# Kernel tuning notes

Hardware: AMD Instinct MI355X
Metric: run time of the kernel (lower is better)

Reference implementation:

```python
import jax, jax.numpy as jnp
import numpy as np

D, H, COND, MLP_RATIO = 1024, 16, 1024, 4
HD = D // H
DFF = MLP_RATIO * D


def layer_norm(x, w, eps=1e-5):
    xf = x.astype(jnp.float32)
    mu = jnp.mean(xf, axis=-1, keepdims=True)
    var = jnp.mean((xf - mu) ** 2, axis=-1, keepdims=True)
    return (xf - mu) * jax.lax.rsqrt(var + eps) * w


def rms_norm(x, w, eps=1e-6):
    xf = x.astype(jnp.float32)
    rms = jnp.sqrt(jnp.mean(xf * xf, axis=-1, keepdims=True) + eps)
    return (xf / rms * w).astype(x.dtype)


def rotate_half(x):
    x1, x2 = x[..., : x.shape[-1] // 2], x[..., x.shape[-1] // 2:]
    return jnp.concatenate([-x2, x1], axis=-1)


def apply_rope(x, cos, sin):
    return x * cos + rotate_half(x) * sin


def setup_inputs() -> dict:
    key = jax.random.key(0)
    ks = jax.random.split(key, 16)
    B, S = 4, 2048
    pos = jnp.arange(S, dtype=jnp.float32)
    inv = 1.0 / (10000.0 ** (jnp.arange(0, HD, 2, dtype=jnp.float32) / HD))
    freqs = pos[:, None] * inv[None, :]              # (S, HD/2)
    emb = jnp.concatenate([freqs, freqs], axis=-1)   # (S, HD)
    return {
        "x": jax.random.normal(ks[0], (B, S, D), jnp.float32),
        "cos": jnp.cos(emb)[None, :, None, :],        # (1,S,1,HD)
        "sin": jnp.sin(emb)[None, :, None, :],
        "c": jax.random.normal(ks[1], (B, COND), jnp.float32),
        "norm1_w": jnp.ones((D,), jnp.float32),
        "Wqkv": jax.random.normal(ks[2], (D, 3 * D), jnp.float32) * 0.02,
        "Wout": jax.random.normal(ks[3], (D, D), jnp.float32) * 0.02,
        "q_norm_w": jnp.ones((HD,), jnp.float32),
        "k_norm_w": jnp.ones((HD,), jnp.float32),
        "norm2_w": jnp.ones((D,), jnp.float32),
        "W1": jax.random.normal(ks[4], (D, DFF), jnp.float32) * 0.02,
        "b1": jnp.zeros((DFF,), jnp.float32),
        "W2": jax.random.normal(ks[5], (DFF, D), jnp.float32) * 0.02,
        "b2": jnp.zeros((D,), jnp.float32),
        "ada_W": jax.random.normal(ks[6], (COND, 6 * D), jnp.float32) * 0.02,
        "ada_b": jnp.zeros((6 * D,), jnp.float32),
    }


def reference(x, cos, sin, c, norm1_w, Wqkv, Wout, q_norm_w, k_norm_w,
              norm2_w, W1, b1, W2, b2, ada_W, ada_b):
    B, S, _ = x.shape
    mod = (c @ ada_W + ada_b)[:, None, :]            # (B,1,6D)
    sh_msa, sc_msa, g_msa, sh_mlp, sc_mlp, g_mlp = jnp.split(mod, 6, axis=-1)

    x_norm = layer_norm(x, norm1_w) * (1 + sc_msa) + sh_msa
    qkv = (x_norm @ Wqkv).reshape(B, S, 3, H, HD)
    q, k, v = qkv[:, :, 0], qkv[:, :, 1], qkv[:, :, 2]  # (B,S,H,HD)
    q = apply_rope(rms_norm(q, q_norm_w), cos, sin)
    k = apply_rope(rms_norm(k, k_norm_w), cos, sin)

    scale = 1.0 / jnp.sqrt(jnp.float32(HD))
    logits = jnp.einsum('bqhd,bkhd->bhqk', q, k) * scale
    probs = jax.nn.softmax(logits, axis=-1)
    attn = jnp.einsum('bhqk,bkhd->bqhd', probs, v).reshape(B, S, D)

    x = x + g_msa * (attn @ Wout)

    x_norm = layer_norm(x, norm2_w) * (1 + sc_mlp) + sh_mlp
    h = jax.nn.gelu(x_norm @ W1 + b1, approximate=True)
    x = x + g_mlp * (h @ W2 + b2)
    return x
```

## Files before the change

kernel.cpp:

```cpp
#include <hip/hip_runtime.h>
#include <hip/hip_bf16.h>
#include <math.h>

typedef __bf16 bf16;
typedef __bf16 bf16x8 __attribute__((ext_vector_type(8)));
typedef __bf16 bf16x4 __attribute__((ext_vector_type(4)));
typedef float f32x4 __attribute__((ext_vector_type(4)));
typedef short s16x4 __attribute__((ext_vector_type(4)));

#define S_LEN 2048
#define NTOK 8192
#define DIM 1024
#define NH 16
#define HEADD 64
#define DFF 4096
#define MODD 6144

__device__ __forceinline__ void gload_lds16(const bf16* g, bf16* l) {
  __builtin_amdgcn_global_load_lds(
      (const __attribute__((address_space(1))) void*)g,
      (__attribute__((address_space(3))) void*)l, 16, 0, 0);
}

__device__ __forceinline__ float gelu_tanh(float x) {
  float inner = 0.7978845608028654f * (x + 0.044715f * x * x * x);
  return 0.5f * x * (1.0f + tanhf(inner));
}

__global__ __launch_bounds__(256) void init_mod_kernel(
    const float* __restrict__ ada_b, float* __restrict__ mod) {
  int i = blockIdx.x * 256 + threadIdx.x;
  mod[i] = ada_b[i % MODD];
}

__global__ __launch_bounds__(256) void ada_gemm_kernel(
    const float* __restrict__ cnd, const float* __restrict__ W,
    float* __restrict__ mod) {
  int n = blockIdx.x * 256 + threadIdx.x;
  int k0 = blockIdx.y * 128;
  float a0 = 0.f, a1 = 0.f, a2 = 0.f, a3 = 0.f;
  for (int k = k0; k < k0 + 128; ++k) {
    float w = W[(size_t)k * MODD + n];
    a0 = fmaf(cnd[k], w, a0);
    a1 = fmaf(cnd[1024 + k], w, a1);
    a2 = fmaf(cnd[2048 + k], w, a2);
    a3 = fmaf(cnd[3072 + k], w, a3);
  }
  atomicAdd(&mod[n], a0);
  atomicAdd(&mod[MODD + n], a1);
  atomicAdd(&mod[2 * MODD + n], a2);
  atomicAdd(&mod[3 * MODD + n], a3);
}

__global__ __launch_bounds__(256) void transpose_cast_kernel(
    const float* __restrict__ W, bf16* __restrict__ Wt, int K, int N) {
  __shared__ float tile[32][33];
  int n0 = blockIdx.x * 32, k0 = blockIdx.y * 32;
  int r = threadIdx.x >> 3;
  int c4 = (threadIdx.x & 7) * 4;
  float4 v = *(const float4*)&W[(size_t)(k0 + r) * N + n0 + c4];
  tile[r][c4 + 0] = v.x; tile[r][c4 + 1] = v.y;
  tile[r][c4 + 2] = v.z; tile[r][c4 + 3] = v.w;
  __syncthreads();
  bf16x4 o;
  o[0] = (bf16)tile[c4 + 0][r];
  o[1] = (bf16)tile[c4 + 1][r];
  o[2] = (bf16)tile[c4 + 2][r];
  o[3] = (bf16)tile[c4 + 3][r];
  *(bf16x4*)&Wt[(size_t)(n0 + r) * K + k0 + c4] = o;
}

__global__ __launch_bounds__(256) void vtrans_kernel(
    const bf16* __restrict__ qkv, bf16* __restrict__ VT) {
  __shared__ __align__(16) bf16 t[64][72];
  const int bh = blockIdx.y;
  const int b = bh >> 4, h = bh & 15;
  const int s0 = blockIdx.x * 64;
  const int tid = threadIdx.x;
  {
    const int r = tid >> 2;
    const int c = (tid & 3) * 16;
    const bf16* src =
        qkv + (size_t)(b * S_LEN + s0 + r) * 3072 + 2048 + h * 64 + c;
    *(bf16x8*)&t[r][c] = *(const bf16x8*)src;
    *(bf16x8*)&t[r][c + 8] = *(const bf16x8*)(src + 8);
  }
  __syncthreads();
  {
    const int d = tid & 63;
    const int sc = (tid >> 6) * 16;
    bf16x8 o0, o1;
#pragma unroll
    for (int j = 0; j < 8; ++j) o0[j] = t[sc + j][d];
#pragma unroll
    for (int j = 0; j < 8; ++j) o1[j] = t[sc + 8 + j][d];
    bf16* dst = VT + (size_t)(bh * 64 + d) * S_LEN + s0 + sc;
    *(bf16x8*)dst = o0;
    *(bf16x8*)(dst + 8) = o1;
  }
}

__global__ __launch_bounds__(256) void ln_mod_kernel(
    const float* __restrict__ x, const float* __restrict__ w,
    const float* __restrict__ mod, int sh_off, int sc_off,
    bf16* __restrict__ out) {
  __shared__ float red[8];
  const int row = blockIdx.x;
  const int b = row >> 11;
  const int tid = threadIdx.x;
  const float4 v = ((const float4*)(x + (size_t)row * DIM))[tid];
  float s1 = v.x + v.y + v.z + v.w;
  float s2 = v.x * v.x + v.y * v.y + v.z * v.z + v.w * v.w;
  for (int off = 32; off > 0; off >>= 1) {
    s1 += __shfl_down(s1, off, 64);
    s2 += __shfl_down(s2, off, 64);
  }
  const int wid = tid >> 6;
  if ((tid & 63) == 0) { red[wid] = s1; red[4 + wid] = s2; }
  __syncthreads();
  s1 = red[0] + red[1] + red[2] + red[3];
  s2 = red[4] + red[5] + red[6] + red[7];
  const float mu = s1 * (1.0f / DIM);
  const float inv = rsqrtf(s2 * (1.0f / DIM) - mu * mu + 1e-5f);
  const int c = tid * 4;
  const float* mb = mod + (size_t)b * MODD;
  float xs[4] = {v.x, v.y, v.z, v.w};
  bf16x4 o;
#pragma unroll
  for (int j = 0; j < 4; ++j)
    o[j] = (bf16)(((xs[j] - mu) * inv) * w[c + j] * (1.0f + mb[sc_off + c + j]) +
                  mb[sh_off + c + j]);
  *(bf16x4*)(out + (size_t)row * DIM + c) = o;
}

template <int EPI>
__global__ __launch_bounds__(256) void gemm_bt(
    const bf16* __restrict__ A, const bf16* __restrict__ Bt,
    bf16* __restrict__ Cb, float* __restrict__ Cf,
    const float* __restrict__ bias, const float* __restrict__ gmod,
    const float* __restrict__ resid, int M, int N, int K) {
  __shared__ __align__(16) bf16 As[2][128 * 32];
  __shared__ __align__(16) bf16 Bs[2][128 * 32];
  const int tid = threadIdx.x;
  const int wid = tid >> 6;
  const int lane = tid & 63;
  const int l15 = lane & 15;
  const int quad = lane >> 4;
  const int m0 = blockIdx.y * 128;
  const int n0 = blockIdx.x * 128;
  const int wm = (wid & 1) * 64;
  const int wn = (wid >> 1) * 64;

  const int r0 = tid >> 2;
  const int cc0 = (tid & 3) * 8;
  const size_t a_base = (size_t)(m0 + r0) * K + cc0;
  const size_t a_base2 = (size_t)(m0 + 64 + r0) * K + cc0;
  const size_t b_base = (size_t)(n0 + r0) * K + cc0;
  const size_t b_base2 = (size_t)(n0 + 64 + r0) * K + cc0;

  f32x4 acc[4][4] = {};

  for (int kt = 0; kt < K; kt += 64) {
    gload_lds16(A + a_base + kt, &As[0][tid * 8]);
    gload_lds16(A + a_base2 + kt, &As[0][(256 + tid) * 8]);
    gload_lds16(Bt + b_base + kt, &Bs[0][tid * 8]);
    gload_lds16(Bt + b_base2 + kt, &Bs[0][(256 + tid) * 8]);
    gload_lds16(A + a_base + kt + 32, &As[1][tid * 8]);
    gload_lds16(A + a_base2 + kt + 32, &As[1][(256 + tid) * 8]);
    gload_lds16(Bt + b_base + kt + 32, &Bs[1][tid * 8]);
    gload_lds16(Bt + b_base2 + kt + 32, &Bs[1][(256 + tid) * 8]);
    __syncthreads();
#pragma unroll
    for (int half = 0; half < 2; ++half) {
      bf16x8 af[4], bfr[4];
#pragma unroll
      for (int i = 0; i < 4; ++i) {
        af[i] = *(const bf16x8*)&As[half][(wm + i * 16 + l15) * 32 + quad * 8];
        bfr[i] = *(const bf16x8*)&Bs[half][(wn + i * 16 + l15) * 32 + quad * 8];
      }
#pragma unroll
      for (int i = 0; i < 4; ++i)
#pragma unroll
        for (int j = 0; j < 4; ++j)
          acc[i][j] = __builtin_amdgcn_mfma_f32_16x16x32_bf16(af[i], bfr[j],
                                                              acc[i][j], 0, 0, 0);
    }
    __syncthreads();
  }

#pragma unroll
  for (int i = 0; i < 4; ++i) {
#pragma unroll
    for (int r = 0; r < 4; ++r) {
      const int m = m0 + wm + i * 16 + quad * 4 + r;
#pragma unroll
      for (int j = 0; j < 4; ++j) {
        const int n = n0 + wn + j * 16 + l15;
        float v = acc[i][j][r];
        if (EPI == 0) {
          Cb[(size_t)m * N + n] = (bf16)v;
        } else if (EPI == 1) {
          const int b = m >> 11;
          Cf[(size_t)m * N + n] =
              resid[(size_t)m * N + n] + gmod[(size_t)b * MODD + n] * v;
        } else if (EPI == 2) {
          v += bias[n];
          Cb[(size_t)m * N + n] = (bf16)gelu_tanh(v);
        } else {
          v += bias[n];
          const int b = m >> 11;
          Cf[(size_t)m * N + n] =
              resid[(size_t)m * N + n] + gmod[(size_t)b * MODD + n] * v;
        }
      }
    }
  }
}

__global__ __launch_bounds__(256) void rope_kernel(
    bf16* __restrict__ qkv, const float* __restrict__ cosb,
    const float* __restrict__ sinb, const float* __restrict__ qw,
    const float* __restrict__ kw) {
  const int wid = threadIdx.x >> 6;
  const int lane = threadIdx.x & 63;
  const int inst = blockIdx.x * 4 + wid;
  const int h = inst & (NH - 1);
  const int token = inst >> 4;
  const int s = token & (S_LEN - 1);
  const size_t base = (size_t)token * (3 * DIM) + h * HEADD + lane;
  const float cv = cosb[s * HEADD + lane];
  const float sv = sinb[s * HEADD + lane];
  const float sign = (lane < 32) ? -1.0f : 1.0f;
  {
    float xq = (float)qkv[base];
    float ss = xq * xq;
    for (int off = 1; off < 64; off <<= 1) ss += __shfl_xor(ss, off, 64);
    float rn = rsqrtf(ss * (1.0f / HEADD) + 1e-6f);
    float xn = xq * rn * qw[lane];
    float other = __shfl_xor(xn, 32, 64);
    qkv[base] = (bf16)(xn * cv + sign * other * sv);
  }
  {
    float xk = (float)qkv[base + DIM];
    float ss = xk * xk;
    for (int off = 1; off < 64; off <<= 1) ss += __shfl_xor(ss, off, 64);
    float rn = rsqrtf(ss * (1.0f / HEADD) + 1e-6f);
    float xn = xk * rn * kw[lane];
    float other = __shfl_xor(xn, 32, 64);
    qkv[base + DIM] = (bf16)(xn * cv + sign * other * sv);
  }
}

__global__ __launch_bounds__(256) void attn_kernel(
    const bf16* __restrict__ qkv, const bf16* __restrict__ VT,
    bf16* __restrict__ out) {
  __shared__ __align__(16) bf16 Ks[4096];
  __shared__ __align__(16) bf16 Vs[4096];
  const int bh = blockIdx.y;
  const int b = bh >> 4;
  const int h = bh & 15;
  const int q0 = blockIdx.x * 128;
  const int tid = threadIdx.x;
  const int wid = tid >> 6;
  const int lane = tid & 63;
  const int l15 = lane & 15;
  const int quad = lane >> 4;

  bf16x8 aq[2][2];
#pragma unroll
  for (int i = 0; i < 2; ++i) {
    const int qrow = q0 + wid * 32 + i * 16 + l15;
    const size_t qbase = (size_t)(b * S_LEN + qrow) * (3 * DIM) + h * HEADD;
    aq[i][0] = *(const bf16x8*)(qkv + qbase + quad * 8);
    aq[i][1] = *(const bf16x8*)(qkv + qbase + 32 + quad * 8);
  }

  const int rstage = tid & 63;
  const int kbase = tid >> 6;
  const float cexp = 0.125f * 1.44269504f;

  f32x4 oacc[2][4] = {};
  float psum[2] = {0.f, 0.f};

  for (int kt = 0; kt < S_LEN; kt += 64) {
    __syncthreads();
    const bf16* krow = qkv + (size_t)(b * S_LEN + kt + rstage) * 3072 + DIM + h * HEADD;
    const bf16* vrow = VT + (size_t)(bh * 64 + rstage) * S_LEN + kt;
    const int rsw = rstage & 7;
#pragma unroll
    for (int rr = 0; rr < 2; ++rr) {
      const int ck = kbase + 4 * rr;
      const int sw = ((ck ^ rsw) << 3);
      *(bf16x8*)&Ks[rstage * 64 + sw] = *(const bf16x8*)(krow + ck * 8);
      *(bf16x8*)&Vs[rstage * 64 + sw] = *(const bf16x8*)(vrow + ck * 8);
    }
    __syncthreads();

    f32x4 sc[2][4] = {};
#pragma unroll
    for (int hh = 0; hh < 2; ++hh) {
#pragma unroll
      for (int cc = 0; cc < 4; ++cc) {
        const int row = cc * 16 + l15;
        const bf16x8 kf = *(const bf16x8*)&Ks[row * 64 + (((quad + 4 * hh) ^ (l15 & 7)) << 3)];
#pragma unroll
        for (int i = 0; i < 2; ++i)
          sc[i][cc] = __builtin_amdgcn_mfma_f32_16x16x32_bf16(kf, aq[i][hh],
                                                              sc[i][cc], 0, 0, 0);
      }
    }

    s16x4 pf[2][4];
#pragma unroll
    for (int i = 0; i < 2; ++i)
#pragma unroll
      for (int cc = 0; cc < 4; ++cc) {
        bf16x4 pb;
#pragma unroll
        for (int r = 0; r < 4; ++r) {
          const float p = __builtin_amdgcn_exp2f(fmaf(sc[i][cc][r], cexp, -8.0f));
          psum[i] += p;
          pb[r] = (bf16)p;
        }
        pf[i][cc] = __builtin_bit_cast(s16x4, pb);
      }

#pragma unroll
    for (int j = 0; j < 4; ++j) {
      const int d = 16 * j + l15;
      const int drow = d * 64;
      const int dsw = d & 7;
#pragma unroll
      for (int cc = 0; cc < 4; ++cc) {
        const int ck = 2 * cc + (quad >> 1);
        const s16x4 vf = *(const s16x4*)&Vs[drow + ((ck ^ dsw) << 3) + ((quad & 1) << 2)];
#pragma unroll
        for (int i = 0; i < 2; ++i)
          oacc[i][j] = __builtin_amdgcn_mfma_f32_16x16x16bf16_1k(pf[i][cc], vf,
                                                                 oacc[i][j], 0, 0, 0);
      }
    }
  }

#pragma unroll
  for (int i = 0; i < 2; ++i) {
    float ps = psum[i];
    ps += __shfl_xor(ps, 16, 64);
    ps += __shfl_xor(ps, 32, 64);
#pragma unroll
    for (int r = 0; r < 4; ++r) {
      const float invl = 1.0f / __shfl(ps, quad * 4 + r, 64);
      const int m = q0 + wid * 32 + i * 16 + quad * 4 + r;
#pragma unroll
      for (int j = 0; j < 4; ++j)
        out[((size_t)(b * S_LEN + m) * NH + h) * HEADD + j * 16 + l15] =
            (bf16)(oacc[i][j][r] * invl);
    }
  }
}

extern "C" void kernel_launch(void* const* d_in, const int* in_sizes, int n_in,
                              void* d_out, int out_size, void* d_ws,
                              size_t ws_size, hipStream_t stream) {
  const float* x = (const float*)d_in[0];
  const float* cosb = (const float*)d_in[1];
  const float* sinb = (const float*)d_in[2];
  const float* cnd = (const float*)d_in[3];
  const float* norm1_w = (const float*)d_in[4];
  const float* Wqkv = (const float*)d_in[5];
  const float* Wout = (const float*)d_in[6];
  const float* q_norm_w = (const float*)d_in[7];
  const float* k_norm_w = (const float*)d_in[8];
  const float* norm2_w = (const float*)d_in[9];
  const float* W1 = (const float*)d_in[10];
  const float* b1 = (const float*)d_in[11];
  const float* W2 = (const float*)d_in[12];
  const float* b2 = (const float*)d_in[13];
  const float* ada_W = (const float*)d_in[14];
  const float* ada_b = (const float*)d_in[15];
  float* out = (float*)d_out;

  char* p = (char*)d_ws;
  float* mod = (float*)p;   p += (size_t)4 * MODD * 4;
  bf16* WqkvT = (bf16*)p;   p += (size_t)3072 * 1024 * 2;
  bf16* WoutT = (bf16*)p;   p += (size_t)1024 * 1024 * 2;
  bf16* W1T = (bf16*)p;     p += (size_t)4096 * 1024 * 2;
  bf16* W2T = (bf16*)p;     p += (size_t)1024 * 4096 * 2;
  bf16* XN = (bf16*)p;      p += (size_t)NTOK * DIM * 2;
  bf16* QKV = (bf16*)p;     p += (size_t)NTOK * 3 * DIM * 2;
  bf16* ATTN = (bf16*)p;    p += (size_t)NTOK * DIM * 2;
  bf16* Hbuf = (bf16*)p;    p += (size_t)NTOK * DFF * 2;
  bf16* VT = Hbuf;

  init_mod_kernel<<<96, 256, 0, stream>>>(ada_b, mod);
  ada_gemm_kernel<<<dim3(24, 8), 256, 0, stream>>>(cnd, ada_W, mod);
  transpose_cast_kernel<<<dim3(96, 32), 256, 0, stream>>>(Wqkv, WqkvT, 1024, 3072);
  transpose_cast_kernel<<<dim3(32, 32), 256, 0, stream>>>(Wout, WoutT, 1024, 1024);
  transpose_cast_kernel<<<dim3(128, 32), 256, 0, stream>>>(W1, W1T, 1024, 4096);
  transpose_cast_kernel<<<dim3(32, 128), 256, 0, stream>>>(W2, W2T, 4096, 1024);
  ln_mod_kernel<<<NTOK, 256, 0, stream>>>(x, norm1_w, mod, 0, 1024, XN);
  gemm_bt<0><<<dim3(24, 64), 256, 0, stream>>>(XN, WqkvT, QKV, nullptr, nullptr,
                                               nullptr, nullptr, NTOK, 3072, 1024);
  rope_kernel<<<NTOK * NH / 4, 256, 0, stream>>>(QKV, cosb, sinb, q_norm_w, k_norm_w);
  vtrans_kernel<<<dim3(32, 64), 256, 0, stream>>>(QKV, VT);
  attn_kernel<<<dim3(16, 64), 256, 0, stream>>>(QKV, VT, ATTN);
  gemm_bt<1><<<dim3(8, 64), 256, 0, stream>>>(ATTN, WoutT, nullptr, out, nullptr,
                                              mod + 2 * 1024, x, NTOK, 1024, 1024);
  ln_mod_kernel<<<NTOK, 256, 0, stream>>>(out, norm2_w, mod, 3 * 1024, 4 * 1024, XN);
  gemm_bt<2><<<dim3(32, 64), 256, 0, stream>>>(XN, W1T, Hbuf, nullptr, b1, nullptr,
                                               nullptr, NTOK, DFF, 1024);
  gemm_bt<3><<<dim3(8, 64), 256, 0, stream>>>(Hbuf, W2T, nullptr, out, b2,
                                              mod + 5 * 1024, out, NTOK, 1024, DFF);
  (void)in_sizes; (void)n_in; (void)out_size; (void)ws_size;
}
```

Before: 681.4 us.

## Fuse QK-norm and RoPE into QKV GEMM, split-K attention, 64-row tiles for N=1024 GEMMs

Moves the per-head RMS norm and RoPE into the QKV GEMM epilogue, which removes the separate rope kernel and its read-modify-write pass over Q/K. Attention is split into two key halves run as separate blocks, with the next K/V tile prefetched into registers. A new reduce kernel sums the unnormalised partial outputs and softmax sums. The Wout and W2 GEMMs use 64-row M tiles to launch more blocks. Partial outputs are stored in bf16 without max subtraction, so precision and scratch traffic both add cost and risk.

```diff
diff --git a/kernel.cpp b/kernel.cpp
--- a/kernel.cpp
+++ b/kernel.cpp
@@ -133,22 +133,25 @@
   *(bf16x4*)(out + (size_t)row * DIM + c) = o;
 }
 
-template <int EPI>
+template <int EPI, int MT>
 __global__ __launch_bounds__(256) void gemm_bt(
     const bf16* __restrict__ A, const bf16* __restrict__ Bt,
     bf16* __restrict__ Cb, float* __restrict__ Cf,
     const float* __restrict__ bias, const float* __restrict__ gmod,
-    const float* __restrict__ resid, int M, int N, int K) {
-  __shared__ __align__(16) bf16 As[2][128 * 32];
+    const float* __restrict__ resid, const float* __restrict__ cosb,
+    const float* __restrict__ sinb, const float* __restrict__ qw,
+    const float* __restrict__ kw, int M, int N, int K) {
+  constexpr int IM = MT / 32;
+  __shared__ __align__(16) bf16 As[2][MT * 32];
   __shared__ __align__(16) bf16 Bs[2][128 * 32];
   const int tid = threadIdx.x;
   const int wid = tid >> 6;
   const int lane = tid & 63;
   const int l15 = lane & 15;
   const int quad = lane >> 4;
-  const int m0 = blockIdx.y * 128;
+  const int m0 = blockIdx.y * MT;
   const int n0 = blockIdx.x * 128;
-  const int wm = (wid & 1) * 64;
+  const int wm = (wid & 1) * (MT / 2);
   const int wn = (wid >> 1) * 64;
 
   const int r0 = tid >> 2;
@@ -158,28 +161,29 @@
   const size_t b_base = (size_t)(n0 + r0) * K + cc0;
   const size_t b_base2 = (size_t)(n0 + 64 + r0) * K + cc0;
 
-  f32x4 acc[4][4] = {};
+  f32x4 acc[IM][4] = {};
 
   for (int kt = 0; kt < K; kt += 64) {
     gload_lds16(A + a_base + kt, &As[0][tid * 8]);
-    gload_lds16(A + a_base2 + kt, &As[0][(256 + tid) * 8]);
+    if (MT == 128) gload_lds16(A + a_base2 + kt, &As[0][(256 + tid) * 8]);
     gload_lds16(Bt + b_base + kt, &Bs[0][tid * 8]);
     gload_lds16(Bt + b_base2 + kt, &Bs[0][(256 + tid) * 8]);
     gload_lds16(A + a_base + kt + 32, &As[1][tid * 8]);
-    gload_lds16(A + a_base2 + kt + 32, &As[1][(256 + tid) * 8]);
+    if (MT == 128) gload_lds16(A + a_base2 + kt + 32, &As[1][(256 + tid) * 8]);
     gload_lds16(Bt + b_base + kt + 32, &Bs[1][tid * 8]);
     gload_lds16(Bt + b_base2 + kt + 32, &Bs[1][(256 + tid) * 8]);
     __syncthreads();
 #pragma unroll
     for (int half = 0; half < 2; ++half) {
-      bf16x8 af[4], bfr[4];
-#pragma unroll
-      for (int i = 0; i < 4; ++i) {
+      bf16x8 af[IM], bfr[4];
+#pragma unroll
+      for (int i = 0; i < IM; ++i)
         af[i] = *(const bf16x8*)&As[half][(wm + i * 16 + l15) * 32 + quad * 8];
-        bfr[i] = *(const bf16x8*)&Bs[half][(wn + i * 16 + l15) * 32 + quad * 8];
-      }
-#pragma unroll
-      for (int i = 0; i < 4; ++i)
+#pragma unroll
+      for (int j = 0; j < 4; ++j)
+        bfr[j] = *(const bf16x8*)&Bs[half][(wn + j * 16 + l15) * 32 + quad * 8];
+#pragma unroll
+      for (int i = 0; i < IM; ++i)
 #pragma unroll
         for (int j = 0; j < 4; ++j)
           acc[i][j] = __builtin_amdgcn_mfma_f32_16x16x32_bf16(af[i], bfr[j],
@@ -188,8 +192,43 @@
     __syncthreads();
   }
 
-#pragma unroll
-  for (int i = 0; i < 4; ++i) {
+  if (EPI == 4 && n0 < 2048) {
+    const float* nw = ((n0 + wn) < 1024) ? qw : kw;
+    float wv[4];
+#pragma unroll
+    for (int j = 0; j < 4; ++j) wv[j] = nw[j * 16 + l15];
+#pragma unroll
+    for (int i = 0; i < IM; ++i) {
+#pragma unroll
+      for (int r = 0; r < 4; ++r) {
+        const int m = m0 + wm + i * 16 + quad * 4 + r;
+        const int s = m & (S_LEN - 1);
+        float v[4];
+        float ss = 0.f;
+#pragma unroll
+        for (int j = 0; j < 4; ++j) { v[j] = acc[i][j][r]; ss += v[j] * v[j]; }
+        ss += __shfl_xor(ss, 1, 64);
+        ss += __shfl_xor(ss, 2, 64);
+        ss += __shfl_xor(ss, 4, 64);
+        ss += __shfl_xor(ss, 8, 64);
+        const float inv = rsqrtf(ss * (1.0f / HEADD) + 1e-6f);
+        float xn[4];
+#pragma unroll
+        for (int j = 0; j < 4; ++j) xn[j] = v[j] * inv * wv[j];
+#pragma unroll
+        for (int j = 0; j < 4; ++j) {
+          const int d = j * 16 + l15;
+          const float rot = (j < 2) ? -xn[j + 2] : xn[j - 2];
+          const float o = xn[j] * cosb[s * HEADD + d] + rot * sinb[s * HEADD + d];
+          Cb[(size_t)m * N + n0 + wn + d] = (bf16)o;
+        }
+      }
+    }
+    return;
+  }
+
+#pragma unroll
+  for (int i = 0; i < IM; ++i) {
 #pragma unroll
     for (int r = 0; r < 4; ++r) {
       const int m = m0 + wm + i * 16 + quad * 4 + r;
@@ -197,7 +236,7 @@
       for (int j = 0; j < 4; ++j) {
         const int n = n0 + wn + j * 16 + l15;
         float v = acc[i][j][r];
-        if (EPI == 0) {
+        if (EPI == 0 || EPI == 4) {
           Cb[(size_t)m * N + n] = (bf16)v;
         } else if (EPI == 1) {
           const int b = m >> 11;
@@ -217,49 +256,16 @@
   }
 }
 
-__global__ __launch_bounds__(256) void rope_kernel(
-    bf16* __restrict__ qkv, const float* __restrict__ cosb,
-    const float* __restrict__ sinb, const float* __restrict__ qw,
-    const float* __restrict__ kw) {
-  const int wid = threadIdx.x >> 6;
-  const int lane = threadIdx.x & 63;
-  const int inst = blockIdx.x * 4 + wid;
-  const int h = inst & (NH - 1);
-  const int token = inst >> 4;
-  const int s = token & (S_LEN - 1);
-  const size_t base = (size_t)token * (3 * DIM) + h * HEADD + lane;
-  const float cv = cosb[s * HEADD + lane];
-  const float sv = sinb[s * HEADD + lane];
-  const float sign = (lane < 32) ? -1.0f : 1.0f;
-  {
-    float xq = (float)qkv[base];
-    float ss = xq * xq;
-    for (int off = 1; off < 64; off <<= 1) ss += __shfl_xor(ss, off, 64);
-    float rn = rsqrtf(ss * (1.0f / HEADD) + 1e-6f);
-    float xn = xq * rn * qw[lane];
-    float other = __shfl_xor(xn, 32, 64);
-    qkv[base] = (bf16)(xn * cv + sign * other * sv);
-  }
-  {
-    float xk = (float)qkv[base + DIM];
-    float ss = xk * xk;
-    for (int off = 1; off < 64; off <<= 1) ss += __shfl_xor(ss, off, 64);
-    float rn = rsqrtf(ss * (1.0f / HEADD) + 1e-6f);
-    float xn = xk * rn * kw[lane];
-    float other = __shfl_xor(xn, 32, 64);
-    qkv[base + DIM] = (bf16)(xn * cv + sign * other * sv);
-  }
-}
-
 __global__ __launch_bounds__(256) void attn_kernel(
     const bf16* __restrict__ qkv, const bf16* __restrict__ VT,
-    bf16* __restrict__ out) {
+    bf16* __restrict__ Opart, float* __restrict__ psumbuf) {
   __shared__ __align__(16) bf16 Ks[4096];
   __shared__ __align__(16) bf16 Vs[4096];
   const int bh = blockIdx.y;
   const int b = bh >> 4;
   const int h = bh & 15;
   const int q0 = blockIdx.x * 128;
+  const int split = blockIdx.z;
   const int tid = threadIdx.x;
   const int wid = tid >> 6;
   const int lane = tid & 63;
@@ -275,26 +281,44 @@
     aq[i][1] = *(const bf16x8*)(qkv + qbase + 32 + quad * 8);
   }
 
-  const int rstage = tid & 63;
-  const int kbase = tid >> 6;
+  const int rstage = lane;
+  const int rsw = rstage & 7;
+  const bf16* krow =
+      qkv + (size_t)(b * S_LEN + split * 1024 + rstage) * 3072 + DIM + h * HEADD;
+  const bf16* vrow = VT + (size_t)(bh * 64 + rstage) * S_LEN + split * 1024;
+
+  bf16x8 kreg[2], vreg[2];
+#pragma unroll
+  for (int rr = 0; rr < 2; ++rr) {
+    const int ck = wid + 4 * rr;
+    kreg[rr] = *(const bf16x8*)(krow + ck * 8);
+    vreg[rr] = *(const bf16x8*)(vrow + ck * 8);
+  }
+
   const float cexp = 0.125f * 1.44269504f;
-
   f32x4 oacc[2][4] = {};
   float psum[2] = {0.f, 0.f};
 
-  for (int kt = 0; kt < S_LEN; kt += 64) {
+  for (int t = 0; t < 16; ++t) {
     __syncthreads();
-    const bf16* krow = qkv + (size_t)(b * S_LEN + kt + rstage) * 3072 + DIM + h * HEADD;
-    const bf16* vrow = VT + (size_t)(bh * 64 + rstage) * S_LEN + kt;
-    const int rsw = rstage & 7;
 #pragma unroll
     for (int rr = 0; rr < 2; ++rr) {
-      const int ck = kbase + 4 * rr;
+      const int ck = wid + 4 * rr;
       const int sw = ((ck ^ rsw) << 3);
-      *(bf16x8*)&Ks[rstage * 64 + sw] = *(const bf16x8*)(krow + ck * 8);
-      *(bf16x8*)&Vs[rstage * 64 + sw] = *(const bf16x8*)(vrow + ck * 8);
+      *(bf16x8*)&Ks[rstage * 64 + sw] = kreg[rr];
+      *(bf16x8*)&Vs[rstage * 64 + sw] = vreg[rr];
     }
     __syncthreads();
+    if (t < 15) {
+      krow += 64 * 3072;
+      vrow += 64;
+#pragma unroll
+      for (int rr = 0; rr < 2; ++rr) {
+        const int ck = wid + 4 * rr;
+        kreg[rr] = *(const bf16x8*)(krow + ck * 8);
+        vreg[rr] = *(const bf16x8*)(vrow + ck * 8);
+      }
+    }
 
     f32x4 sc[2][4] = {};
 #pragma unroll
@@ -302,7 +326,8 @@
 #pragma unroll
       for (int cc = 0; cc < 4; ++cc) {
         const int row = cc * 16 + l15;
-        const bf16x8 kf = *(const bf16x8*)&Ks[row * 64 + (((quad + 4 * hh) ^ (l15 & 7)) << 3)];
+        const bf16x8 kf =
+            *(const bf16x8*)&Ks[row * 64 + (((quad + 4 * hh) ^ (l15 & 7)) << 3)];
 #pragma unroll
         for (int i = 0; i < 2; ++i)
           sc[i][cc] = __builtin_amdgcn_mfma_f32_16x16x32_bf16(kf, aq[i][hh],
@@ -333,7 +358,8 @@
 #pragma unroll
       for (int cc = 0; cc < 4; ++cc) {
         const int ck = 2 * cc + (quad >> 1);
-        const s16x4 vf = *(const s16x4*)&Vs[drow + ((ck ^ dsw) << 3) + ((quad & 1) << 2)];
+        const s16x4 vf =
+            *(const s16x4*)&Vs[drow + ((ck ^ dsw) << 3) + ((quad & 1) << 2)];
 #pragma unroll
         for (int i = 0; i < 2; ++i)
           oacc[i][j] = __builtin_amdgcn_mfma_f32_16x16x16bf16_1k(pf[i][cc], vf,
@@ -347,16 +373,40 @@
     float ps = psum[i];
     ps += __shfl_xor(ps, 16, 64);
     ps += __shfl_xor(ps, 32, 64);
+    if (lane < 16) {
+      const int qrow = q0 + wid * 32 + i * 16 + lane;
+      psumbuf[(size_t)split * (NTOK * NH) + (size_t)(b * S_LEN + qrow) * NH + h] = ps;
+    }
 #pragma unroll
     for (int r = 0; r < 4; ++r) {
-      const float invl = 1.0f / __shfl(ps, quad * 4 + r, 64);
       const int m = q0 + wid * 32 + i * 16 + quad * 4 + r;
 #pragma unroll
       for (int j = 0; j < 4; ++j)
-        out[((size_t)(b * S_LEN + m) * NH + h) * HEADD + j * 16 + l15] =
-            (bf16)(oacc[i][j][r] * invl);
-    }
-  }
+        Opart[(size_t)split * (NTOK * DIM) +
+              ((size_t)(b * S_LEN + m) * NH + h) * HEADD + j * 16 + l15] =
+            (bf16)oacc[i][j][r];
+    }
+  }
+}
+
+__global__ __launch_bounds__(256) void attn_reduce_kernel(
+    const bf16* __restrict__ Opart, const float* __restrict__ psumbuf,
+    bf16* __restrict__ attn) {
+  const int g = blockIdx.x * 256 + threadIdx.x;
+  const int token = g >> 7;
+  const int rem = g & 127;
+  const int h = rem >> 3;
+  const int d0 = (rem & 7) * 8;
+  const size_t off = ((size_t)token * NH + h) * HEADD + d0;
+  const bf16x8 o0 = *(const bf16x8*)(Opart + off);
+  const bf16x8 o1 = *(const bf16x8*)(Opart + (size_t)NTOK * DIM + off);
+  const float l = psumbuf[token * NH + h] + psumbuf[NTOK * NH + token * NH + h];
+  const float invl = 1.0f / l;
+  bf16x8 o;
+#pragma unroll
+  for (int j = 0; j < 8; ++j)
+    o[j] = (bf16)(((float)o0[j] + (float)o1[j]) * invl);
+  *(bf16x8*)(attn + off) = o;
 }
 
 extern "C" void kernel_launch(void* const* d_in, const int* in_sizes, int n_in,
@@ -391,6 +441,8 @@
   bf16* ATTN = (bf16*)p;    p += (size_t)NTOK * DIM * 2;
   bf16* Hbuf = (bf16*)p;    p += (size_t)NTOK * DFF * 2;
   bf16* VT = Hbuf;
+  bf16* Opart = Hbuf + (size_t)NTOK * DIM;
+  float* psumbuf = (float*)(Hbuf + (size_t)3 * NTOK * DIM);
 
   init_mod_kernel<<<96, 256, 0, stream>>>(ada_b, mod);
   ada_gemm_kernel<<<dim3(24, 8), 256, 0, stream>>>(cnd, ada_W, mod);
@@ -399,17 +451,21 @@
   transpose_cast_kernel<<<dim3(128, 32), 256, 0, stream>>>(W1, W1T, 1024, 4096);
   transpose_cast_kernel<<<dim3(32, 128), 256, 0, stream>>>(W2, W2T, 4096, 1024);
   ln_mod_kernel<<<NTOK, 256, 0, stream>>>(x, norm1_w, mod, 0, 1024, XN);
-  gemm_bt<0><<<dim3(24, 64), 256, 0, stream>>>(XN, WqkvT, QKV, nullptr, nullptr,
-                                               nullptr, nullptr, NTOK, 3072, 1024);
-  rope_kernel<<<NTOK * NH / 4, 256, 0, stream>>>(QKV, cosb, sinb, q_norm_w, k_norm_w);
+  gemm_bt<4, 128><<<dim3(24, 64), 256, 0, stream>>>(
+      XN, WqkvT, QKV, nullptr, nullptr, nullptr, nullptr, cosb, sinb,
+      q_norm_w, k_norm_w, NTOK, 3072, 1024);
   vtrans_kernel<<<dim3(32, 64), 256, 0, stream>>>(QKV, VT);
-  attn_kernel<<<dim3(16, 64), 256, 0, stream>>>(QKV, VT, ATTN);
-  gemm_bt<1><<<dim3(8, 64), 256, 0, stream>>>(ATTN, WoutT, nullptr, out, nullptr,
-                                              mod + 2 * 1024, x, NTOK, 1024, 1024);
+  attn_kernel<<<dim3(16, 64, 2), 256, 0, stream>>>(QKV, VT, Opart, psumbuf);
+  attn_reduce_kernel<<<4096, 256, 0, stream>>>(Opart, psumbuf, ATTN);
+  gemm_bt<1, 64><<<dim3(8, 128), 256, 0, stream>>>(
+      ATTN, WoutT, nullptr, out, nullptr, mod + 2 * 1024, x, nullptr, nullptr,
+      nullptr, nullptr, NTOK, 1024, 1024);
   ln_mod_kernel<<<NTOK, 256, 0, stream>>>(out, norm2_w, mod, 3 * 1024, 4 * 1024, XN);
-  gemm_bt<2><<<dim3(32, 64), 256, 0, stream>>>(XN, W1T, Hbuf, nullptr, b1, nullptr,
-                                               nullptr, NTOK, DFF, 1024);
-  gemm_bt<3><<<dim3(8, 64), 256, 0, stream>>>(Hbuf, W2T, nullptr, out, b2,
-                                              mod + 5 * 1024, out, NTOK, 1024, DFF);
+  gemm_bt<2, 128><<<dim3(32, 64), 256, 0, stream>>>(
+      XN, W1T, Hbuf, nullptr, b1, nullptr, nullptr, nullptr, nullptr,
+      nullptr, nullptr, NTOK, DFF, 1024);
+  gemm_bt<3, 64><<<dim3(8, 128), 256, 0, stream>>>(
+      Hbuf, W2T, nullptr, out, b2, mod + 5 * 1024, out, nullptr, nullptr,
+      nullptr, nullptr, NTOK, 1024, DFF);
   (void)in_sizes; (void)n_in; (void)out_size; (void)ws_size;
 }
```

Measured after the change: 667.1 us. -2.1%, faster.
